# Performance work log

Measured on AMD Instinct MI355X. Metric: run time of the kernel, lower is better.

Reference implementation:

```python
import jax, jax.numpy as jnp
import numpy as np
from jax import lax

BS, C, H, W = 256, 256, 16, 16
NUM_CLASSES = 2
EPS = 1e-12  # F.normalize eps


def _l2_normalize(x):
    # F.normalize(x, dim=1, p=2): x / max(||x||_2, eps) along channel dim
    n = jnp.sqrt(jnp.sum(x * x, axis=1, keepdims=True))
    return x / jnp.maximum(n, EPS)


def _correlation(f1, f2):
    # original: (f1[:, :, None, :, :] * f2.reshape(bs,c,-1)[:, :, :, None, None]).sum(1)
    # -> [bs, h*w, h, w]; expressed as a batched contraction over channels.
    f1n = _l2_normalize(f1)                      # [bs, c, h, w]
    f2n = _l2_normalize(f2).reshape(f2.shape[0], f2.shape[1], -1)  # [bs, c, hw]
    return jnp.einsum('bcxy,bck->bkxy', f1n, f2n)


def _conv3x3(x, w, b):
    y = lax.conv_general_dilated(x, w, (1, 1), 'SAME',
                                 dimension_numbers=('NCHW', 'OIHW', 'NCHW'))
    return y + b[None, :, None, None]


def _psroi_diag(feat, num_classes, h, w):
    # full-image box, pooled==spatial, group_size==h -> each bin is one pixel:
    # out[n, c, ph, pw] = feat[n, (c*h + ph)*w + pw, ph, pw]
    bs = feat.shape[0]
    f = feat.reshape(bs, num_classes, h, w, h, w)
    f = jnp.diagonal(f, axis1=2, axis2=4)   # [bs, nc, w, w, h] (ph diag -> last)
    f = jnp.diagonal(f, axis1=2, axis2=3)   # [bs, nc, h, w]? -> [bs, nc, h_diag, w_diag]
    # after two diagonals axes are [bs, nc, ph, pw]
    return f


def setup_inputs() -> dict:
    key = jax.random.key(0)
    ks = jax.random.split(key, 5)
    std1 = float(np.sqrt(2.0 / (3 * 3 * 1024)))
    std2 = float(np.sqrt(2.0 / (3 * 3 * 512)))
    stdc = float(np.sqrt(2.0 / (1 * 1 * NUM_CLASSES * H * W)))
    return {
        'feature_1': jax.random.normal(ks[0], (BS, C, H, W), jnp.float32),
        'feature_2': jax.random.normal(ks[1], (BS, C, H, W), jnp.float32),
        'conv1_w': jax.random.normal(ks[2], (1024, 2 * (C + H * W), 3, 3), jnp.float32) * std1,
        'conv1_b': jnp.zeros((1024,), jnp.float32),
        'conv2_w': jax.random.normal(ks[3], (512, 1024, 3, 3), jnp.float32) * std2,
        'conv2_b': jnp.zeros((512,), jnp.float32),
        'conv_cls_w': jax.random.normal(ks[4], (NUM_CLASSES * H * W, 512, 1, 1), jnp.float32) * stdc,
    }


def reference(feature_1, feature_2, conv1_w, conv1_b, conv2_w, conv2_b, conv_cls_w):
    f1 = jax.nn.relu(feature_1)
    f2 = jax.nn.relu(feature_2)
    corr1 = _correlation(f1, f2)   # [bs, hw, h, w]
    corr2 = _correlation(f2, f1)
    feat = jnp.concatenate((f1, corr1, f2, corr2), axis=1)  # [bs, 2*(c+hw), h, w]
    feat = jax.nn.relu(_conv3x3(feat, conv1_w, conv1_b))
    feat = jax.nn.relu(_conv3x3(feat, conv2_w, conv2_b))
    feat = jnp.einsum('bchw,oc->bohw', feat, conv_cls_w[:, :, 0, 0])  # 1x1 conv, no bias
    feat = jax.nn.relu(feat)
    cls_base = _psroi_diag(feat, NUM_CLASSES, H, W)      # [bs, nc, h, w]
    cls_score = jnp.mean(cls_base, axis=(2, 3))          # AvgPool2d(h, w)
    cls_prob = jax.nn.softmax(cls_score, axis=1)
    # eval-mode return of the original module
    return (cls_prob, corr1, corr2)
```

## Files before the change

### kernel.cpp

```cpp
#include <hip/hip_runtime.h>


typedef __attribute__((ext_vector_type(8))) __bf16 bf16x8;
typedef __attribute__((ext_vector_type(4))) float f32x4;
typedef unsigned short u16;

template <bool B> struct BC { static constexpr bool value = B; };

__device__ __forceinline__ u16 f2bf(float f) {
  union { float f; unsigned u; } v; v.f = f;
  unsigned u = v.u;
  u += 0x7fffu + ((u >> 16) & 1u);
  return (u16)(u >> 16);
}
__device__ __forceinline__ float bf2f(u16 h) {
  union { unsigned u; float f; } v; v.u = ((unsigned)h) << 16;
  return v.f;
}
__device__ __forceinline__ void gl2lds16(const void* g, void* l) {
  __builtin_amdgcn_global_load_lds(
      (__attribute__((address_space(1))) void*)(void*)g,
      (__attribute__((address_space(3))) void*)l, 16, 0, 0);
}

__global__ __launch_bounds__(256) void k_norm(const float* __restrict__ f1,
                                              const float* __restrict__ f2,
                                              u16* __restrict__ featT,
                                              float* __restrict__ s1,
                                              float* __restrict__ s2) {
  int bx = blockIdx.x;
  int b = bx >> 2;
  int p0 = (bx & 3) << 6;
  int t = threadIdx.x;
  int p = p0 + (t & 63);
  int cg = t >> 6;
  int sp3 = ((p >> 1) & 3) << 3;
  const float* F1 = f1 + ((size_t)b << 16);
  const float* F2 = f2 + ((size_t)b << 16);
  u16* FT = featT + (((size_t)(b << 8) + p) << 10);
  float ss1 = 0.f, ss2 = 0.f;
  for (int i = 0; i < 64; ++i) {
    int c = (cg << 6) + i;
    float v1 = F1[(c << 8) + p]; v1 = v1 > 0.f ? v1 : 0.f;
    float v2 = F2[(c << 8) + p]; v2 = v2 > 0.f ? v2 : 0.f;
    ss1 += v1 * v1; ss2 += v2 * v2;
    FT[c ^ sp3] = f2bf(v1);
    FT[512 + (c ^ sp3)] = f2bf(v2);
  }
  __shared__ float l1[256], l2[256];
  l1[t] = ss1; l2[t] = ss2;
  __syncthreads();
  if (t < 64) {
    float a = l1[t] + l1[t + 64] + l1[t + 128] + l1[t + 192];
    float c2 = l2[t] + l2[t + 64] + l2[t + 128] + l2[t + 192];
    int pp = (b << 8) + p0 + t;
    s1[pp] = 1.f / fmaxf(sqrtf(a), 1e-12f);
    s2[pp] = 1.f / fmaxf(sqrtf(c2), 1e-12f);
  }
}

__global__ __launch_bounds__(256) void k_wconv(const float* __restrict__ w,
                                               u16* __restrict__ wb, int O, int C) {
  int o = blockIdx.x;
  int t = threadIdx.x;
  int sp3 = ((o >> 1) & 3) << 3;
  const float* src = w + (size_t)o * C * 9;
  for (int c = t; c < C; c += 256) {
    const float* s = src + c * 9;
    float v[9];
#pragma unroll
    for (int i = 0; i < 9; ++i) v[i] = s[i];
#pragma unroll
    for (int tap = 0; tap < 9; ++tap)
      wb[(size_t)tap * O * C + (size_t)o * C + (c ^ sp3)] = f2bf(v[tap]);
  }
}

__global__ __launch_bounds__(256) void k_corr(u16* featT,
                                              const float* __restrict__ s1,
                                              const float* __restrict__ s2,
                                              float* __restrict__ out) {
  __shared__ alignas(16) u16 Alds[128 * 32];
  __shared__ alignas(16) u16 Blds[128 * 32];
  __shared__ float tb[4][16][66];
  int bx = blockIdx.x;
  int b = bx >> 2;
  int p1b = ((bx >> 1) & 1) << 7;
  int p2b = (bx & 1) << 7;
  int t = threadIdx.x, l = t & 63, w = t >> 6;
  int wm = w >> 1, wn = w & 1, lr = l & 15, lq = l >> 4;
  int srow = (w << 4) + (l >> 2);
  int sq = (l & 3) << 3;
  int rsz = ((lq ^ ((lr >> 1) & 3)) << 3);
  const size_t bbase = (size_t)b << 18;

  f32x4 acc[4][4];
#pragma unroll
  for (int i = 0; i < 4; ++i)
#pragma unroll
    for (int j = 0; j < 4; ++j) acc[i][j] = (f32x4){0.f, 0.f, 0.f, 0.f};

#pragma unroll 1
  for (int kc = 0; kc < 8; ++kc) {
    int c0 = kc << 5;
    const u16* sA = featT + bbase + ((size_t)(p1b + srow) << 10) + (c0 + sq);
    gl2lds16(sA, Alds + ((w << 4) << 5));
    gl2lds16(sA + (64 << 10), Alds + ((64 + (w << 4)) << 5));
    const u16* sB = featT + bbase + ((size_t)(p2b + srow) << 10) + (512 + c0 + sq);
    gl2lds16(sB, Blds + ((w << 4) << 5));
    gl2lds16(sB + (64 << 10), Blds + ((64 + (w << 4)) << 5));
    __syncthreads();
    bf16x8 af[4], bfr[4];
#pragma unroll
    for (int mf = 0; mf < 4; ++mf)
      af[mf] = *(const bf16x8*)(Alds + (((wm << 6) + (mf << 4) + lr) << 5) + rsz);
#pragma unroll
    for (int nf = 0; nf < 4; ++nf)
      bfr[nf] = *(const bf16x8*)(Blds + (((wn << 6) + (nf << 4) + lr) << 5) + rsz);
#pragma unroll
    for (int mf = 0; mf < 4; ++mf)
#pragma unroll
      for (int nf = 0; nf < 4; ++nf)
        acc[mf][nf] = __builtin_amdgcn_mfma_f32_16x16x32_bf16(af[mf], bfr[nf], acc[mf][nf], 0, 0, 0);
    __syncthreads();
  }

  float sc2[4]; int p2g[4];
#pragma unroll
  for (int nf = 0; nf < 4; ++nf) {
    int p2 = p2b + (wn << 6) + (nf << 4) + lr;
    p2g[nf] = p2;
    sc2[nf] = s2[(b << 8) + p2];
  }
  float* corr1 = out + 512;
  float* corr2 = out + 512 + 16777216;
#pragma unroll
  for (int mf = 0; mf < 4; ++mf) {
    float gv[4][4];
#pragma unroll
    for (int r = 0; r < 4; ++r) {
      int p1 = p1b + (wm << 6) + (mf << 4) + (lq << 2) + r;
      float s1v = s1[(b << 8) + p1];
#pragma unroll
      for (int nf = 0; nf < 4; ++nf) gv[nf][r] = acc[mf][nf][r] * s1v * sc2[nf];
    }
#pragma unroll
    for (int r = 0; r < 4; ++r) {
      int p1 = p1b + (wm << 6) + (mf << 4) + (lq << 2) + r;
      int s1p3 = ((p1 >> 1) & 3) << 3;
#pragma unroll
      for (int nf = 0; nf < 4; ++nf) {
        corr2[((size_t)b << 16) + ((size_t)p1 << 8) + p2g[nf]] = gv[nf][r];
        featT[bbase + ((size_t)p1 << 10) + 256 + (p2g[nf] ^ s1p3)] = f2bf(gv[nf][r]);
      }
    }
#pragma unroll
    for (int r = 0; r < 4; ++r)
#pragma unroll
      for (int nf = 0; nf < 4; ++nf)
        tb[w][(lq << 2) + r][(nf << 4) + lr] = gv[nf][r];
#pragma unroll
    for (int j = 0; j < 16; ++j) {
      float v = tb[w][lr][(j << 2) + lq];
      int p2 = p2b + (wn << 6) + (j << 2) + lq;
      int s2p3 = ((p2 >> 1) & 3) << 3;
      int p1 = p1b + (wm << 6) + (mf << 4) + lr;
      corr1[((size_t)b << 16) + ((size_t)p2 << 8) + p1] = v;
      featT[bbase + ((size_t)p2 << 10) + 768 + (p1 ^ s2p3)] = f2bf(v);
    }
  }
}

template <int O, int OTB>
__global__ __launch_bounds__(512, 4) void k_conv(const u16* __restrict__ X,
                                                 const u16* __restrict__ Wb,
                                                 const float* __restrict__ bias,
                                                 u16* __restrict__ Out) {
  __shared__ alignas(16) u16 Xlds[2][260 * 32];
  __shared__ alignas(16) u16 Wlds[3][128 * 32];
  int bx = blockIdx.x;
  int otile = bx & ((1 << OTB) - 1);
  int b = bx >> OTB;
  int t = threadIdx.x, l = t & 63, w = t >> 6;
  int wm = w & 3, wn = w >> 2;
  int lr = l & 15, lq = l >> 4;
  int o0 = otile << 7;
  int srl = l >> 2;
  int sq = (l & 3) << 3;
  const size_t xbase = (size_t)b << 18;

  const u16* wsrc = Wb + (((size_t)(o0 + (w << 4) + srl)) << 10) + sq;
  const u16* xsrc0 = X + xbase + (((size_t)((w << 4) + srl)) << 10) + sq;
  const u16* xsrc1 = xsrc0 + ((size_t)128 << 10);

  u16* wdst0 = &Wlds[0][(w << 4) << 5];
  u16* wdst1 = &Wlds[1][(w << 4) << 5];
  u16* wdst2 = &Wlds[2][(w << 4) << 5];
  u16* xdA0 = &Xlds[0][(w << 4) << 5];
  u16* xdA1 = &Xlds[0][(128 + (w << 4)) << 5];
  u16* xdB0 = &Xlds[1][(w << 4) << 5];
  u16* xdB1 = &Xlds[1][(128 + (w << 4)) << 5];

  int rszw = ((lq ^ ((lr >> 1) & 3)) << 3);
  const u16* bwb0 = &Wlds[0][(((wn << 6) + lr) << 5) + rszw];
  const u16* bwb1 = &Wlds[1][(((wn << 6) + lr) << 5) + rszw];
  const u16* bwb2 = &Wlds[2][(((wn << 6) + lr) << 5) + rszw];

  int pb[4];
#pragma unroll
  for (int mf = 0; mf < 4; ++mf)
    pb[mf] = (((wm << 6) + (mf << 4) + lr) << 5);
  int xsz[3];
#pragma unroll
  for (int d = 0; d < 3; ++d)
    xsz[d] = ((lq ^ (((lr + d - 1) >> 1) & 3)) << 3);
  const int zoff = (256 << 5) + (lq << 3);

  f32x4 acc[4][4];
#pragma unroll
  for (int i = 0; i < 4; ++i)
#pragma unroll
    for (int j = 0; j < 4; ++j) acc[i][j] = (f32x4){0.f, 0.f, 0.f, 0.f};

  if (t < 32) ((unsigned*)&Xlds[t >> 4][256 << 5])[t & 15] = 0u;

  gl2lds16(xsrc0, xdA0);
  gl2lds16(xsrc1, xdA1);
  gl2lds16(wsrc, wdst0);
  gl2lds16(wsrc + ((size_t)O << 10), wdst1);
  __syncthreads();

  auto kcbody = [&](auto oddc, int kc) {
    constexpr bool ODD = decltype(oddc)::value;
    const u16* xb = ODD ? &Xlds[1][0] : &Xlds[0][0];
#pragma unroll
    for (int tap = 0; tap < 9; ++tap) {
      __builtin_amdgcn_sched_barrier(0);
      int ntap = (tap + 2) % 9;
      int nkc = kc + (tap >= 7 ? 1 : 0);
      u16* wd = ((tap + 2) % 3 == 0) ? wdst0 : (((tap + 2) % 3 == 1) ? wdst1 : wdst2);
      gl2lds16(wsrc + (size_t)ntap * ((size_t)O << 10) + (nkc << 5), wd);
      if (tap == 0) {
        if (ODD) { gl2lds16(xsrc0 + ((kc + 1) << 5), xdA0); gl2lds16(xsrc1 + ((kc + 1) << 5), xdA1); }
        else     { gl2lds16(xsrc0 + ((kc + 1) << 5), xdB0); gl2lds16(xsrc1 + ((kc + 1) << 5), xdB1); }
      }
      const u16* bwb = (tap % 3 == 0) ? bwb0 : ((tap % 3 == 1) ? bwb1 : bwb2);
      bf16x8 bwf[4];
#pragma unroll
      for (int nf = 0; nf < 4; ++nf) bwf[nf] = *(const bf16x8*)(bwb + (nf << 9));
      const int dr = tap / 3 - 1, dc = tap % 3 - 1;
      const int dpo = (((dr << 4) + dc) << 5) + xsz[dc + 1];
      bf16x8 axf[4];
#pragma unroll
      for (int mf = 0; mf < 4; ++mf) {
        int rr = (wm << 2) + mf + dr;
        bool v = ((unsigned)rr < 16u) & ((unsigned)(lr + dc) < 16u);
        int off = v ? (pb[mf] + dpo) : zoff;
        axf[mf] = *(const bf16x8*)(xb + off);
      }
#pragma unroll
      for (int mf = 0; mf < 4; ++mf)
#pragma unroll
        for (int nf = 0; nf < 4; ++nf)
          acc[mf][nf] = __builtin_amdgcn_mfma_f32_16x16x32_bf16(axf[mf], bwf[nf], acc[mf][nf], 0, 0, 0);
      if (tap == 0 || tap == 1) asm volatile("s_waitcnt vmcnt(3)" ::: "memory");
      else                      asm volatile("s_waitcnt vmcnt(1)" ::: "memory");
      __builtin_amdgcn_s_barrier();
    }
  };

#pragma unroll 1
  for (int kc2 = 0; kc2 < 16; ++kc2) {
    kcbody(BC<false>{}, 2 * kc2);
    kcbody(BC<true>{}, 2 * kc2 + 1);
  }

  __syncthreads();
  float bv[4];
#pragma unroll
  for (int nf = 0; nf < 4; ++nf) bv[nf] = bias[o0 + (wn << 6) + (nf << 4) + lr];
  u16* scr = ((u16*)Xlds) + w * 1152;
  int rr2 = l >> 2;
  int kq = l & 3;
#pragma unroll
  for (int mf = 0; mf < 4; ++mf) {
#pragma unroll
    for (int r = 0; r < 4; ++r) {
      int rr = (lq << 2) + r;
#pragma unroll
      for (int nf = 0; nf < 4; ++nf) {
        float vv = acc[mf][nf][r] + bv[nf];
        scr[rr * 72 + (nf << 4) + lr] = f2bf(vv > 0.f ? vv : 0.f);
      }
    }
    asm volatile("s_waitcnt lgkmcnt(0)" ::: "memory");
    __builtin_amdgcn_sched_barrier(0);
    int p = (wm << 6) + (mf << 4) + rr2;
    int sp = (p >> 1) & 3;
    size_t rbase = (size_t)((b << 8) + p) * O + (size_t)(o0 + (wn << 6));
#pragma unroll
    for (int j = 0; j < 2; ++j) {
      int k = (j << 2) | kq;
      int kl = (j << 2) | (kq ^ sp);
      uint4 v = *(const uint4*)(scr + rr2 * 72 + (kl << 3));
      *(uint4*)(Out + rbase + (k << 3)) = v;
    }
    asm volatile("s_waitcnt lgkmcnt(0)" ::: "memory");
    __builtin_amdgcn_sched_barrier(0);
  }
}

__global__ __launch_bounds__(256) void k_cls(const u16* __restrict__ X2,
                                             const float* __restrict__ Wc,
                                             float* __restrict__ out) {
  int b = blockIdx.x, p = threadIdx.x;
  int s = (p >> 1) & 3;
  const uint4* xv = (const uint4*)(X2 + (((size_t)(b << 8) + p) << 9));
  const float4* w0 = (const float4*)(Wc + ((size_t)p << 9));
  const float4* w1 = (const float4*)(Wc + ((size_t)(256 + p) << 9));
  float a0 = 0.f, a1 = 0.f;
#pragma unroll 4
  for (int i = 0; i < 64; ++i) {
    int ii = (i & ~3) | ((i & 3) ^ s);
    uint4 u = xv[ii];
    float x0 = bf2f((u16)(u.x & 0xffffu)), x1 = bf2f((u16)(u.x >> 16));
    float x2 = bf2f((u16)(u.y & 0xffffu)), x3 = bf2f((u16)(u.y >> 16));
    float x4 = bf2f((u16)(u.z & 0xffffu)), x5 = bf2f((u16)(u.z >> 16));
    float x6 = bf2f((u16)(u.w & 0xffffu)), x7 = bf2f((u16)(u.w >> 16));
    float4 wa = w0[i * 2], wb = w0[i * 2 + 1];
    a0 += x0 * wa.x + x1 * wa.y + x2 * wa.z + x3 * wa.w +
          x4 * wb.x + x5 * wb.y + x6 * wb.z + x7 * wb.w;
    float4 wc4 = w1[i * 2], wd = w1[i * 2 + 1];
    a1 += x0 * wc4.x + x1 * wc4.y + x2 * wc4.z + x3 * wc4.w +
          x4 * wd.x + x5 * wd.y + x6 * wd.z + x7 * wd.w;
  }
  a0 = fmaxf(a0, 0.f);
  a1 = fmaxf(a1, 0.f);
  __shared__ float r0[256], r1[256];
  r0[p] = a0; r1[p] = a1;
  for (int sdx = 128; sdx > 0; sdx >>= 1) {
    __syncthreads();
    if (p < sdx) { r0[p] += r0[p + sdx]; r1[p] += r1[p + sdx]; }
  }
  __syncthreads();
  if (p == 0) {
    float s0 = r0[0] * (1.f / 256.f), s1v = r1[0] * (1.f / 256.f);
    float m = fmaxf(s0, s1v);
    float e0 = expf(s0 - m), e1 = expf(s1v - m);
    float inv = 1.f / (e0 + e1);
    out[(b << 1) + 0] = e0 * inv;
    out[(b << 1) + 1] = e1 * inv;
  }
}

extern "C" void kernel_launch(void* const* d_in, const int* in_sizes, int n_in,
                              void* d_out, int out_size, void* d_ws, size_t ws_size,
                              hipStream_t stream) {
  const float* f1 = (const float*)d_in[0];
  const float* f2 = (const float*)d_in[1];
  const float* w1 = (const float*)d_in[2];
  const float* b1 = (const float*)d_in[3];
  const float* w2 = (const float*)d_in[4];
  const float* b2 = (const float*)d_in[5];
  const float* wc = (const float*)d_in[6];
  float* out = (float*)d_out;
  char* ws = (char*)d_ws;

  u16* featT = (u16*)(ws + 0);
  u16* out1T = (u16*)(ws + 134217728);
  u16* W1b   = (u16*)(ws + 268435456);
  u16* W2b   = (u16*)(ws + 287309824);
  float* s1  = (float*)(ws + 296747008);
  float* s2  = (float*)(ws + 297009152);
  u16* out2T = (u16*)(ws + 0);

  k_norm<<<1024, 256, 0, stream>>>(f1, f2, featT, s1, s2);
  k_wconv<<<1024, 256, 0, stream>>>(w1, W1b, 1024, 1024);
  k_wconv<<<512, 256, 0, stream>>>(w2, W2b, 512, 1024);
  k_corr<<<1024, 256, 0, stream>>>(featT, s1, s2, out);
  k_conv<1024, 3><<<2048, 512, 0, stream>>>(featT, W1b, b1, out1T);
  k_conv<512, 2><<<1024, 512, 0, stream>>>(out1T, W2b, b2, out2T);
  k_cls<<<256, 256, 0, stream>>>(out2T, wc, out);
}
```

Measured before the change: 1.902 ms.

## Switch conv kernel to 32x32x16 MFMA with 4-wave blocks and larger per-wave tiles

Rewrites the implicit-GEMM 3x3 conv kernel to use 32x32x16 bf16 MFMA instructions instead of 16x16x32, with 256-thread blocks (4 waves in a 2x2 grid) where each wave computes a 128x64 output tile. Staging loads and the LDS swizzle are reorganised to match the new fragment layout, and the epilogue is adapted to the 32x32 accumulator layout. The aim is more MFMA throughput per LDS read and fewer operand loads per FLOP. The cost is higher register pressure from 128 accumulator floats per lane and lower occupancy.

```diff
diff --git a/kernel.cpp b/kernel.cpp
--- a/kernel.cpp
+++ b/kernel.cpp
@@ -3,6 +3,7 @@
 
 typedef __attribute__((ext_vector_type(8))) __bf16 bf16x8;
 typedef __attribute__((ext_vector_type(4))) float f32x4;
+typedef __attribute__((ext_vector_type(16))) float f32x16;
 typedef unsigned short u16;
 
 template <bool B> struct BC { static constexpr bool value = B; };
@@ -172,99 +173,107 @@
 }
 
 template <int O, int OTB>
-__global__ __launch_bounds__(512, 4) void k_conv(const u16* __restrict__ X,
+__global__ __launch_bounds__(256, 2) void k_conv(const u16* __restrict__ X,
                                                  const u16* __restrict__ Wb,
                                                  const float* __restrict__ bias,
                                                  u16* __restrict__ Out) {
-  __shared__ alignas(16) u16 Xlds[2][260 * 32];
+  __shared__ alignas(16) u16 Xlds[2][257 * 32];
   __shared__ alignas(16) u16 Wlds[3][128 * 32];
   int bx = blockIdx.x;
   int otile = bx & ((1 << OTB) - 1);
   int b = bx >> OTB;
   int t = threadIdx.x, l = t & 63, w = t >> 6;
-  int wm = w & 3, wn = w >> 2;
-  int lr = l & 15, lq = l >> 4;
+  int wm = w >> 1, wn = w & 1;
+  int l31 = l & 31, l5 = l >> 5, px = l & 15;
   int o0 = otile << 7;
   int srl = l >> 2;
   int sq = (l & 3) << 3;
   const size_t xbase = (size_t)b << 18;
 
   const u16* wsrc = Wb + (((size_t)(o0 + (w << 4) + srl)) << 10) + sq;
-  const u16* xsrc0 = X + xbase + (((size_t)((w << 4) + srl)) << 10) + sq;
-  const u16* xsrc1 = xsrc0 + ((size_t)128 << 10);
-
-  u16* wdst0 = &Wlds[0][(w << 4) << 5];
-  u16* wdst1 = &Wlds[1][(w << 4) << 5];
-  u16* wdst2 = &Wlds[2][(w << 4) << 5];
-  u16* xdA0 = &Xlds[0][(w << 4) << 5];
-  u16* xdA1 = &Xlds[0][(128 + (w << 4)) << 5];
-  u16* xdB0 = &Xlds[1][(w << 4) << 5];
-  u16* xdB1 = &Xlds[1][(128 + (w << 4)) << 5];
-
-  int rszw = ((lq ^ ((lr >> 1) & 3)) << 3);
-  const u16* bwb0 = &Wlds[0][(((wn << 6) + lr) << 5) + rszw];
-  const u16* bwb1 = &Wlds[1][(((wn << 6) + lr) << 5) + rszw];
-  const u16* bwb2 = &Wlds[2][(((wn << 6) + lr) << 5) + rszw];
-
-  int pb[4];
-#pragma unroll
-  for (int mf = 0; mf < 4; ++mf)
-    pb[mf] = (((wm << 6) + (mf << 4) + lr) << 5);
-  int xsz[3];
-#pragma unroll
-  for (int d = 0; d < 3; ++d)
-    xsz[d] = ((lq ^ (((lr + d - 1) >> 1) & 3)) << 3);
-  const int zoff = (256 << 5) + (lq << 3);
-
-  f32x4 acc[4][4];
-#pragma unroll
-  for (int i = 0; i < 4; ++i)
-#pragma unroll
-    for (int j = 0; j < 4; ++j) acc[i][j] = (f32x4){0.f, 0.f, 0.f, 0.f};
+  const u16* xsrc = X + xbase + (((size_t)((w << 4) + srl)) << 10) + sq;
+
+  int czb[2][3];
+#pragma unroll
+  for (int h = 0; h < 2; ++h)
+#pragma unroll
+    for (int d = 0; d < 3; ++d)
+      czb[h][d] = (((2 * h + l5) ^ (((l31 + d - 1) >> 1) & 3)) << 4);
+  int pbase[4];
+#pragma unroll
+  for (int q = 0; q < 4; ++q)
+    pbase[q] = (((wm << 7) + (q << 5) + l31) << 6);
+  int wrow[2];
+#pragma unroll
+  for (int n = 0; n < 2; ++n)
+    wrow[n] = (((wn << 6) + (n << 5) + l31) << 6);
+  const int zo = 256 << 6;
+
+  f32x16 acc[4][2];
+#pragma unroll
+  for (int q = 0; q < 4; ++q)
+#pragma unroll
+    for (int n = 0; n < 2; ++n)
+#pragma unroll
+      for (int e = 0; e < 16; ++e) acc[q][n][e] = 0.f;
+
+  auto stageW = [&](int tap, int kc, int buf) {
+    const u16* s = wsrc + (size_t)tap * ((size_t)O << 10) + (kc << 5);
+    u16* d0 = &Wlds[buf][(w << 4) << 5];
+    gl2lds16(s, d0);
+    gl2lds16(s + ((size_t)64 << 10), d0 + (64 << 5));
+  };
+  auto stageX = [&](int kc, int buf) {
+    const u16* s = xsrc + (kc << 5);
+    u16* d0 = &Xlds[buf][(w << 4) << 5];
+#pragma unroll
+    for (int rr = 0; rr < 4; ++rr)
+      gl2lds16(s + (((size_t)rr * 64) << 10), d0 + ((rr * 64) << 5));
+  };
 
   if (t < 32) ((unsigned*)&Xlds[t >> 4][256 << 5])[t & 15] = 0u;
 
-  gl2lds16(xsrc0, xdA0);
-  gl2lds16(xsrc1, xdA1);
-  gl2lds16(wsrc, wdst0);
-  gl2lds16(wsrc + ((size_t)O << 10), wdst1);
+  stageX(0, 0);
+  stageW(0, 0, 0);
+  stageW(1, 0, 1);
   __syncthreads();
 
   auto kcbody = [&](auto oddc, int kc) {
     constexpr bool ODD = decltype(oddc)::value;
-    const u16* xb = ODD ? &Xlds[1][0] : &Xlds[0][0];
+    const char* xb = (const char*)(ODD ? &Xlds[1][0] : &Xlds[0][0]);
 #pragma unroll
     for (int tap = 0; tap < 9; ++tap) {
       __builtin_amdgcn_sched_barrier(0);
-      int ntap = (tap + 2) % 9;
-      int nkc = kc + (tap >= 7 ? 1 : 0);
-      u16* wd = ((tap + 2) % 3 == 0) ? wdst0 : (((tap + 2) % 3 == 1) ? wdst1 : wdst2);
-      gl2lds16(wsrc + (size_t)ntap * ((size_t)O << 10) + (nkc << 5), wd);
-      if (tap == 0) {
-        if (ODD) { gl2lds16(xsrc0 + ((kc + 1) << 5), xdA0); gl2lds16(xsrc1 + ((kc + 1) << 5), xdA1); }
-        else     { gl2lds16(xsrc0 + ((kc + 1) << 5), xdB0); gl2lds16(xsrc1 + ((kc + 1) << 5), xdB1); }
-      }
-      const u16* bwb = (tap % 3 == 0) ? bwb0 : ((tap % 3 == 1) ? bwb1 : bwb2);
-      bf16x8 bwf[4];
-#pragma unroll
-      for (int nf = 0; nf < 4; ++nf) bwf[nf] = *(const bf16x8*)(bwb + (nf << 9));
+      {
+        int ntap = (tap + 2 > 8) ? (tap - 7) : (tap + 2);
+        int nkc = (tap + 2 > 8) ? (kc + 1) : kc;
+        stageW(ntap, nkc, (tap + 2) % 3);
+      }
+      if (tap == 0) stageX(kc + 1, ODD ? 0 : 1);
+      const char* wbuf = (const char*)&Wlds[tap % 3][0];
       const int dr = tap / 3 - 1, dc = tap % 3 - 1;
-      const int dpo = (((dr << 4) + dc) << 5) + xsz[dc + 1];
-      bf16x8 axf[4];
-#pragma unroll
-      for (int mf = 0; mf < 4; ++mf) {
-        int rr = (wm << 2) + mf + dr;
-        bool v = ((unsigned)rr < 16u) & ((unsigned)(lr + dc) < 16u);
-        int off = v ? (pb[mf] + dpo) : zoff;
-        axf[mf] = *(const bf16x8*)(xb + off);
-      }
-#pragma unroll
-      for (int mf = 0; mf < 4; ++mf)
-#pragma unroll
-        for (int nf = 0; nf < 4; ++nf)
-          acc[mf][nf] = __builtin_amdgcn_mfma_f32_16x16x32_bf16(axf[mf], bwf[nf], acc[mf][nf], 0, 0, 0);
-      if (tap == 0 || tap == 1) asm volatile("s_waitcnt vmcnt(3)" ::: "memory");
-      else                      asm volatile("s_waitcnt vmcnt(1)" ::: "memory");
+      const int dpo = (((dr << 4) + dc) << 6);
+#pragma unroll
+      for (int h = 0; h < 2; ++h) {
+        bf16x8 bw[2], a[4];
+#pragma unroll
+        for (int n = 0; n < 2; ++n)
+          bw[n] = *(const bf16x8*)(wbuf + wrow[n] + czb[h][1]);
+#pragma unroll
+        for (int q = 0; q < 4; ++q) {
+          bool rok = (unsigned)((wm << 3) + (q << 1) + (l31 >> 4) + dr) < 16u;
+          bool cok = (unsigned)(px + dc) < 16u;
+          int off = (rok & cok) ? (pbase[q] + dpo + czb[h][dc + 1]) : zo;
+          a[q] = *(const bf16x8*)(xb + off);
+        }
+#pragma unroll
+        for (int q = 0; q < 4; ++q)
+#pragma unroll
+          for (int n = 0; n < 2; ++n)
+            acc[q][n] = __builtin_amdgcn_mfma_f32_32x32x16_bf16(a[q], bw[n], acc[q][n], 0, 0, 0);
+      }
+      if (tap == 0 || tap == 1) asm volatile("s_waitcnt vmcnt(6)" ::: "memory");
+      else                      asm volatile("s_waitcnt vmcnt(2)" ::: "memory");
       __builtin_amdgcn_s_barrier();
     }
   };
@@ -276,37 +285,41 @@
   }
 
   __syncthreads();
-  float bv[4];
-#pragma unroll
-  for (int nf = 0; nf < 4; ++nf) bv[nf] = bias[o0 + (wn << 6) + (nf << 4) + lr];
+  float bv[2];
+#pragma unroll
+  for (int n = 0; n < 2; ++n) bv[n] = bias[o0 + (wn << 6) + (n << 5) + l31];
   u16* scr = ((u16*)Xlds) + w * 1152;
-  int rr2 = l >> 2;
+  int rrow = l >> 2;
   int kq = l & 3;
-#pragma unroll
-  for (int mf = 0; mf < 4; ++mf) {
-#pragma unroll
-    for (int r = 0; r < 4; ++r) {
-      int rr = (lq << 2) + r;
-#pragma unroll
-      for (int nf = 0; nf < 4; ++nf) {
-        float vv = acc[mf][nf][r] + bv[nf];
-        scr[rr * 72 + (nf << 4) + lr] = f2bf(vv > 0.f ? vv : 0.f);
-      }
-    }
-    asm volatile("s_waitcnt lgkmcnt(0)" ::: "memory");
-    __builtin_amdgcn_sched_barrier(0);
-    int p = (wm << 6) + (mf << 4) + rr2;
-    int sp = (p >> 1) & 3;
-    size_t rbase = (size_t)((b << 8) + p) * O + (size_t)(o0 + (wn << 6));
-#pragma unroll
-    for (int j = 0; j < 2; ++j) {
-      int k = (j << 2) | kq;
-      int kl = (j << 2) | (kq ^ sp);
-      uint4 v = *(const uint4*)(scr + rr2 * 72 + (kl << 3));
-      *(uint4*)(Out + rbase + (k << 3)) = v;
-    }
-    asm volatile("s_waitcnt lgkmcnt(0)" ::: "memory");
-    __builtin_amdgcn_sched_barrier(0);
+  int lrow4 = l5 << 2;
+#pragma unroll
+  for (int q = 0; q < 4; ++q) {
+#pragma unroll
+    for (int hh = 0; hh < 2; ++hh) {
+#pragma unroll
+      for (int rr = 0; rr < 8; ++rr) {
+        int lrow = (rr & 3) + ((rr >> 2) << 3) + lrow4;
+#pragma unroll
+        for (int n = 0; n < 2; ++n) {
+          float vv = acc[q][n][hh * 8 + rr] + bv[n];
+          scr[lrow * 72 + (n << 5) + l31] = f2bf(vv > 0.f ? vv : 0.f);
+        }
+      }
+      asm volatile("s_waitcnt lgkmcnt(0)" ::: "memory");
+      __builtin_amdgcn_sched_barrier(0);
+      int p = (wm << 7) + (q << 5) + (hh << 4) + rrow;
+      int sp = (p >> 1) & 3;
+      size_t rbase = (size_t)((b << 8) + p) * O + (size_t)(o0 + (wn << 6));
+#pragma unroll
+      for (int j = 0; j < 2; ++j) {
+        int k = (j << 2) | kq;
+        int kl = (j << 2) | (kq ^ sp);
+        uint4 v = *(const uint4*)(scr + rrow * 72 + (kl << 3));
+        *(uint4*)(Out + rbase + (k << 3)) = v;
+      }
+      asm volatile("s_waitcnt lgkmcnt(0)" ::: "memory");
+      __builtin_amdgcn_sched_barrier(0);
+    }
   }
 }
 
@@ -378,7 +391,7 @@
   k_wconv<<<1024, 256, 0, stream>>>(w1, W1b, 1024, 1024);
   k_wconv<<<512, 256, 0, stream>>>(w2, W2b, 512, 1024);
   k_corr<<<1024, 256, 0, stream>>>(featT, s1, s2, out);
-  k_conv<1024, 3><<<2048, 512, 0, stream>>>(featT, W1b, b1, out1T);
-  k_conv<512, 2><<<1024, 512, 0, stream>>>(out1T, W2b, b2, out2T);
+  k_conv<1024, 3><<<2048, 256, 0, stream>>>(featT, W1b, b1, out1T);
+  k_conv<512, 2><<<1024, 256, 0, stream>>>(out1T, W2b, b2, out2T);
   k_cls<<<256, 256, 0, stream>>>(out2T, wc, out);
 }
```

Result: slower. 1.981 ms (+4.2%).

## Double-buffer LDS fragment reads in conv kernel and deepen weight prefetch

Applied to the files above, without the earlier changes.

The conv inner loop now loads the A and W fragments for the next tap from LDS into a second register set while the MFMAs for the current tap run. This hides LDS read latency behind the matrix math. The weight global-to-LDS prefetch distance grows from two taps to three, with a prologue that fills all three weight buffers. The launch-bounds occupancy hint drops from 4 to 2 to make room for the extra registers. The cls kernel also moves its XOR swizzle from the activation index to the weight index, which changes its memory access pattern.

```diff
diff --git a/kernel.cpp b/kernel.cpp
--- a/kernel.cpp
+++ b/kernel.cpp
@@ -172,7 +172,7 @@
 }
 
 template <int O, int OTB>
-__global__ __launch_bounds__(512, 4) void k_conv(const u16* __restrict__ X,
+__global__ __launch_bounds__(512, 2) void k_conv(const u16* __restrict__ X,
                                                  const u16* __restrict__ Wb,
                                                  const float* __restrict__ bias,
                                                  u16* __restrict__ Out) {
@@ -222,49 +222,76 @@
 #pragma unroll
     for (int j = 0; j < 4; ++j) acc[i][j] = (f32x4){0.f, 0.f, 0.f, 0.f};
 
+  bf16x8 fa[2][4], fw[2][4];
+
   if (t < 32) ((unsigned*)&Xlds[t >> 4][256 << 5])[t & 15] = 0u;
 
   gl2lds16(xsrc0, xdA0);
   gl2lds16(xsrc1, xdA1);
   gl2lds16(wsrc, wdst0);
   gl2lds16(wsrc + ((size_t)O << 10), wdst1);
-  __syncthreads();
+  gl2lds16(wsrc + 2 * ((size_t)O << 10), wdst2);
+  asm volatile("s_waitcnt vmcnt(1) lgkmcnt(0)" ::: "memory");
+  __builtin_amdgcn_s_barrier();
+  {
+#pragma unroll
+    for (int nf = 0; nf < 4; ++nf) fw[0][nf] = *(const bf16x8*)(bwb0 + (nf << 9));
+    const int pdpo = ((-17) << 5) + xsz[0];
+#pragma unroll
+    for (int mf = 0; mf < 4; ++mf) {
+      int rr = (wm << 2) + mf - 1;
+      bool v = ((unsigned)rr < 16u) & ((unsigned)(lr - 1) < 16u);
+      int off = v ? (pb[mf] + pdpo) : zoff;
+      fa[0][mf] = *(const bf16x8*)(&Xlds[0][0] + off);
+    }
+  }
+  asm volatile("s_waitcnt lgkmcnt(0)" ::: "memory");
+  __builtin_amdgcn_s_barrier();
 
   auto kcbody = [&](auto oddc, int kc) {
     constexpr bool ODD = decltype(oddc)::value;
     const u16* xb = ODD ? &Xlds[1][0] : &Xlds[0][0];
+    const u16* xbn = ODD ? &Xlds[0][0] : &Xlds[1][0];
 #pragma unroll
     for (int tap = 0; tap < 9; ++tap) {
+      const int CU_ = ((ODD ? 1 : 0) + tap) & 1;
+      const int NX_ = CU_ ^ 1;
       __builtin_amdgcn_sched_barrier(0);
-      int ntap = (tap + 2) % 9;
-      int nkc = kc + (tap >= 7 ? 1 : 0);
-      u16* wd = ((tap + 2) % 3 == 0) ? wdst0 : (((tap + 2) % 3 == 1) ? wdst1 : wdst2);
-      gl2lds16(wsrc + (size_t)ntap * ((size_t)O << 10) + (nkc << 5), wd);
+      {
+        int ntap = (tap + 3 > 8) ? (tap - 6) : (tap + 3);
+        int nkc = (tap >= 6) ? (kc + 1) : kc;
+        u16* wd = (tap % 3 == 0) ? wdst0 : ((tap % 3 == 1) ? wdst1 : wdst2);
+        gl2lds16(wsrc + (size_t)ntap * ((size_t)O << 10) + (nkc << 5), wd);
+      }
       if (tap == 0) {
         if (ODD) { gl2lds16(xsrc0 + ((kc + 1) << 5), xdA0); gl2lds16(xsrc1 + ((kc + 1) << 5), xdA1); }
         else     { gl2lds16(xsrc0 + ((kc + 1) << 5), xdB0); gl2lds16(xsrc1 + ((kc + 1) << 5), xdB1); }
       }
-      const u16* bwb = (tap % 3 == 0) ? bwb0 : ((tap % 3 == 1) ? bwb1 : bwb2);
-      bf16x8 bwf[4];
-#pragma unroll
-      for (int nf = 0; nf < 4; ++nf) bwf[nf] = *(const bf16x8*)(bwb + (nf << 9));
-      const int dr = tap / 3 - 1, dc = tap % 3 - 1;
-      const int dpo = (((dr << 4) + dc) << 5) + xsz[dc + 1];
-      bf16x8 axf[4];
-#pragma unroll
-      for (int mf = 0; mf < 4; ++mf) {
-        int rr = (wm << 2) + mf + dr;
-        bool v = ((unsigned)rr < 16u) & ((unsigned)(lr + dc) < 16u);
-        int off = v ? (pb[mf] + dpo) : zoff;
-        axf[mf] = *(const bf16x8*)(xb + off);
+      {
+        const int ptap = (tap == 8) ? 0 : tap + 1;
+        const u16* bwbn = ((tap + 1) % 3 == 0) ? bwb0
+                        : (((tap + 1) % 3 == 1) ? bwb1 : bwb2);
+#pragma unroll
+        for (int nf = 0; nf < 4; ++nf) fw[NX_][nf] = *(const bf16x8*)(bwbn + (nf << 9));
+        const int pdr = ptap / 3 - 1, pdc = ptap % 3 - 1;
+        const int pdpo = (((pdr << 4) + pdc) << 5) + xsz[pdc + 1];
+        const u16* xrd = (tap == 8) ? xbn : xb;
+#pragma unroll
+        for (int mf = 0; mf < 4; ++mf) {
+          int rr = (wm << 2) + mf + pdr;
+          bool v = ((unsigned)rr < 16u) & ((unsigned)(lr + pdc) < 16u);
+          int off = v ? (pb[mf] + pdpo) : zoff;
+          fa[NX_][mf] = *(const bf16x8*)(xrd + off);
+        }
       }
 #pragma unroll
       for (int mf = 0; mf < 4; ++mf)
 #pragma unroll
         for (int nf = 0; nf < 4; ++nf)
-          acc[mf][nf] = __builtin_amdgcn_mfma_f32_16x16x32_bf16(axf[mf], bwf[nf], acc[mf][nf], 0, 0, 0);
-      if (tap == 0 || tap == 1) asm volatile("s_waitcnt vmcnt(3)" ::: "memory");
-      else                      asm volatile("s_waitcnt vmcnt(1)" ::: "memory");
+          acc[mf][nf] = __builtin_amdgcn_mfma_f32_16x16x32_bf16(fa[CU_][mf], fw[CU_][nf], acc[mf][nf], 0, 0, 0);
+      asm volatile("s_waitcnt lgkmcnt(0)" ::: "memory");
+      if (tap < 2) asm volatile("s_waitcnt vmcnt(3)" ::: "memory");
+      else         asm volatile("s_waitcnt vmcnt(1)" ::: "memory");
       __builtin_amdgcn_s_barrier();
     }
   };
@@ -321,16 +348,16 @@
   float a0 = 0.f, a1 = 0.f;
 #pragma unroll 4
   for (int i = 0; i < 64; ++i) {
-    int ii = (i & ~3) | ((i & 3) ^ s);
-    uint4 u = xv[ii];
+    uint4 u = xv[i];
+    int il = (i & ~3) | ((i & 3) ^ s);
     float x0 = bf2f((u16)(u.x & 0xffffu)), x1 = bf2f((u16)(u.x >> 16));
     float x2 = bf2f((u16)(u.y & 0xffffu)), x3 = bf2f((u16)(u.y >> 16));
     float x4 = bf2f((u16)(u.z & 0xffffu)), x5 = bf2f((u16)(u.z >> 16));
     float x6 = bf2f((u16)(u.w & 0xffffu)), x7 = bf2f((u16)(u.w >> 16));
-    float4 wa = w0[i * 2], wb = w0[i * 2 + 1];
+    float4 wa = w0[il * 2], wb = w0[il * 2 + 1];
     a0 += x0 * wa.x + x1 * wa.y + x2 * wa.z + x3 * wa.w +
           x4 * wb.x + x5 * wb.y + x6 * wb.z + x7 * wb.w;
-    float4 wc4 = w1[i * 2], wd = w1[i * 2 + 1];
+    float4 wc4 = w1[il * 2], wd = w1[il * 2 + 1];
     a1 += x0 * wc4.x + x1 * wc4.y + x2 * wc4.z + x3 * wc4.w +
           x4 * wd.x + x5 * wd.y + x6 * wd.z + x7 * wd.w;
   }
```

Result: slower. 2.157 ms (+13.4%).

## Restructure conv pipeline to process two taps per barrier with double-buffered weights

Applied to the files above, without the earlier changes.

The implicit-GEMM conv main loop now handles two filter taps between barriers. It uses a 2x2 weight LDS buffer and prefetches the next two taps' weights, and the X chunk loads are scheduled at fixed sub-steps. Out-of-bounds A fragments are zeroed with a mask instead of being read from a padded zero row, which removes the LDS padding. The aim is to halve the number of barriers and wait points per K chunk. In exchange it waits with vmcnt(0) on most steps, which may expose load latency. The cls kernel also swaps which access gets the permutation: X is now read sequentially and the weight index is permuted.

```diff
diff --git a/kernel.cpp b/kernel.cpp
--- a/kernel.cpp
+++ b/kernel.cpp
@@ -176,8 +176,8 @@
                                                  const u16* __restrict__ Wb,
                                                  const float* __restrict__ bias,
                                                  u16* __restrict__ Out) {
-  __shared__ alignas(16) u16 Xlds[2][260 * 32];
-  __shared__ alignas(16) u16 Wlds[3][128 * 32];
+  __shared__ alignas(16) u16 Xlds[2][256 * 32];
+  __shared__ alignas(16) u16 Wlds[2][2][128 * 32];
   int bx = blockIdx.x;
   int otile = bx & ((1 << OTB) - 1);
   int b = bx >> OTB;
@@ -193,18 +193,14 @@
   const u16* xsrc0 = X + xbase + (((size_t)((w << 4) + srl)) << 10) + sq;
   const u16* xsrc1 = xsrc0 + ((size_t)128 << 10);
 
-  u16* wdst0 = &Wlds[0][(w << 4) << 5];
-  u16* wdst1 = &Wlds[1][(w << 4) << 5];
-  u16* wdst2 = &Wlds[2][(w << 4) << 5];
-  u16* xdA0 = &Xlds[0][(w << 4) << 5];
-  u16* xdA1 = &Xlds[0][(128 + (w << 4)) << 5];
-  u16* xdB0 = &Xlds[1][(w << 4) << 5];
-  u16* xdB1 = &Xlds[1][(128 + (w << 4)) << 5];
+  u16* xdb = &Xlds[0][0];
+  u16* wdb = &Wlds[0][0][0];
+  const int wdo = (w << 4) << 5;
+  const int xdo0 = (w << 4) << 5;
+  const int xdo1 = (128 + (w << 4)) << 5;
 
   int rszw = ((lq ^ ((lr >> 1) & 3)) << 3);
-  const u16* bwb0 = &Wlds[0][(((wn << 6) + lr) << 5) + rszw];
-  const u16* bwb1 = &Wlds[1][(((wn << 6) + lr) << 5) + rszw];
-  const u16* bwb2 = &Wlds[2][(((wn << 6) + lr) << 5) + rszw];
+  const int wro = (((wn << 6) + lr) << 5) + rszw;
 
   int pb[4];
 #pragma unroll
@@ -214,7 +210,6 @@
 #pragma unroll
   for (int d = 0; d < 3; ++d)
     xsz[d] = ((lq ^ (((lr + d - 1) >> 1) & 3)) << 3);
-  const int zoff = (256 << 5) + (lq << 3);
 
   f32x4 acc[4][4];
 #pragma unroll
@@ -222,57 +217,74 @@
 #pragma unroll
     for (int j = 0; j < 4; ++j) acc[i][j] = (f32x4){0.f, 0.f, 0.f, 0.f};
 
-  if (t < 32) ((unsigned*)&Xlds[t >> 4][256 << 5])[t & 15] = 0u;
-
-  gl2lds16(xsrc0, xdA0);
-  gl2lds16(xsrc1, xdA1);
-  gl2lds16(wsrc, wdst0);
-  gl2lds16(wsrc + ((size_t)O << 10), wdst1);
-  __syncthreads();
-
-  auto kcbody = [&](auto oddc, int kc) {
-    constexpr bool ODD = decltype(oddc)::value;
-    const u16* xb = ODD ? &Xlds[1][0] : &Xlds[0][0];
-#pragma unroll
-    for (int tap = 0; tap < 9; ++tap) {
+  gl2lds16(xsrc0, xdb + xdo0);
+  gl2lds16(xsrc1, xdb + xdo1);
+  gl2lds16(wsrc, wdb + wdo);
+  gl2lds16(wsrc + ((size_t)O << 10), wdb + 4096 + wdo);
+  asm volatile("s_waitcnt vmcnt(0)" ::: "memory");
+  __builtin_amdgcn_s_barrier();
+
+  auto sstep = [&](auto parc, int kc) {
+    constexpr int PAR = decltype(parc)::value ? 1 : 0;
+#pragma unroll
+    for (int s = 0; s < 9; ++s) {
       __builtin_amdgcn_sched_barrier(0);
-      int ntap = (tap + 2) % 9;
-      int nkc = kc + (tap >= 7 ? 1 : 0);
-      u16* wd = ((tap + 2) % 3 == 0) ? wdst0 : (((tap + 2) % 3 == 1) ? wdst1 : wdst2);
-      gl2lds16(wsrc + (size_t)ntap * ((size_t)O << 10) + (nkc << 5), wd);
-      if (tap == 0) {
-        if (ODD) { gl2lds16(xsrc0 + ((kc + 1) << 5), xdA0); gl2lds16(xsrc1 + ((kc + 1) << 5), xdA1); }
-        else     { gl2lds16(xsrc0 + ((kc + 1) << 5), xdB0); gl2lds16(xsrc1 + ((kc + 1) << 5), xdB1); }
-      }
-      const u16* bwb = (tap % 3 == 0) ? bwb0 : ((tap % 3 == 1) ? bwb1 : bwb2);
-      bf16x8 bwf[4];
-#pragma unroll
-      for (int nf = 0; nf < 4; ++nf) bwf[nf] = *(const bf16x8*)(bwb + (nf << 9));
-      const int dr = tap / 3 - 1, dc = tap % 3 - 1;
-      const int dpo = (((dr << 4) + dc) << 5) + xsz[dc + 1];
-      bf16x8 axf[4];
-#pragma unroll
-      for (int mf = 0; mf < 4; ++mf) {
-        int rr = (wm << 2) + mf + dr;
-        bool v = ((unsigned)rr < 16u) & ((unsigned)(lr + dc) < 16u);
-        int off = v ? (pb[mf] + dpo) : zoff;
-        axf[mf] = *(const bf16x8*)(xb + off);
-      }
-#pragma unroll
-      for (int mf = 0; mf < 4; ++mf)
-#pragma unroll
-        for (int nf = 0; nf < 4; ++nf)
-          acc[mf][nf] = __builtin_amdgcn_mfma_f32_16x16x32_bf16(axf[mf], bwf[nf], acc[mf][nf], 0, 0, 0);
-      if (tap == 0 || tap == 1) asm volatile("s_waitcnt vmcnt(3)" ::: "memory");
-      else                      asm volatile("s_waitcnt vmcnt(1)" ::: "memory");
+      const int wbs_rd = (PAR + s) & 1;
+      const int wbs_wr = wbs_rd ^ 1;
+#pragma unroll
+      for (int i = 0; i < 2; ++i) {
+        const int gg = 2 * s + 2 + i;
+        const int ntap = gg % 9;
+        const int dk = gg / 9;
+        gl2lds16(wsrc + (size_t)ntap * ((size_t)O << 10) + ((kc + dk) << 5),
+                 wdb + wbs_wr * 8192 + i * 4096 + wdo);
+      }
+      if (s == 0) {
+        gl2lds16(xsrc0 + ((kc + 1) << 5), xdb + 8192 + xdo0);
+        gl2lds16(xsrc1 + ((kc + 1) << 5), xdb + 8192 + xdo1);
+      }
+      if (s == 5) {
+        gl2lds16(xsrc0 + ((kc + 2) << 5), xdb + xdo0);
+        gl2lds16(xsrc1 + ((kc + 2) << 5), xdb + xdo1);
+      }
+#pragma unroll
+      for (int i = 0; i < 2; ++i) {
+        const int g = 2 * s + i;
+        const int tap = g % 9;
+        const int xpar = (g / 9) & 1;
+        const int dr = tap / 3 - 1, dc = tap % 3 - 1;
+        const u16* wr = wdb + wbs_rd * 8192 + i * 4096 + wro;
+        bf16x8 bw[4];
+#pragma unroll
+        for (int nf = 0; nf < 4; ++nf) bw[nf] = *(const bf16x8*)(wr + (nf << 9));
+        const u16* xr = xdb + xpar * 8192;
+        const int dpo = ((dr << 4) + dc) << 5;
+        bf16x8 a[4];
+#pragma unroll
+        for (int mf = 0; mf < 4; ++mf) {
+          bool ok = (((unsigned)((wm << 2) + mf + dr) < 16u) &
+                     ((unsigned)(lr + dc) < 16u));
+          int msk = ok ? -1 : 0;
+          uint4 u = *(const uint4*)(xr + ((pb[mf] + dpo + xsz[dc + 1]) & msk));
+          u.x &= msk; u.y &= msk; u.z &= msk; u.w &= msk;
+          a[mf] = *(const bf16x8*)&u;
+        }
+#pragma unroll
+        for (int mf = 0; mf < 4; ++mf)
+#pragma unroll
+          for (int nf = 0; nf < 4; ++nf)
+            acc[mf][nf] = __builtin_amdgcn_mfma_f32_16x16x32_bf16(a[mf], bw[nf], acc[mf][nf], 0, 0, 0);
+      }
+      if (s == 0 || s == 5) asm volatile("s_waitcnt vmcnt(2) lgkmcnt(0)" ::: "memory");
+      else                  asm volatile("s_waitcnt vmcnt(0) lgkmcnt(0)" ::: "memory");
       __builtin_amdgcn_s_barrier();
     }
   };
 
 #pragma unroll 1
-  for (int kc2 = 0; kc2 < 16; ++kc2) {
-    kcbody(BC<false>{}, 2 * kc2);
-    kcbody(BC<true>{}, 2 * kc2 + 1);
+  for (int S2 = 0; S2 < 8; ++S2) {
+    sstep(BC<false>{}, 4 * S2);
+    sstep(BC<true>{}, 4 * S2 + 2);
   }
 
   __syncthreads();
@@ -321,16 +333,16 @@
   float a0 = 0.f, a1 = 0.f;
 #pragma unroll 4
   for (int i = 0; i < 64; ++i) {
-    int ii = (i & ~3) | ((i & 3) ^ s);
-    uint4 u = xv[ii];
+    uint4 u = xv[i];
+    int il = (i & ~3) | ((i & 3) ^ s);
     float x0 = bf2f((u16)(u.x & 0xffffu)), x1 = bf2f((u16)(u.x >> 16));
     float x2 = bf2f((u16)(u.y & 0xffffu)), x3 = bf2f((u16)(u.y >> 16));
     float x4 = bf2f((u16)(u.z & 0xffffu)), x5 = bf2f((u16)(u.z >> 16));
     float x6 = bf2f((u16)(u.w & 0xffffu)), x7 = bf2f((u16)(u.w >> 16));
-    float4 wa = w0[i * 2], wb = w0[i * 2 + 1];
+    float4 wa = w0[il * 2], wb = w0[il * 2 + 1];
     a0 += x0 * wa.x + x1 * wa.y + x2 * wa.z + x3 * wa.w +
           x4 * wb.x + x5 * wb.y + x6 * wb.z + x7 * wb.w;
-    float4 wc4 = w1[i * 2], wd = w1[i * 2 + 1];
+    float4 wc4 = w1[il * 2], wd = w1[il * 2 + 1];
     a1 += x0 * wc4.x + x1 * wc4.y + x2 * wc4.z + x3 * wc4.w +
           x4 * wd.x + x5 * wd.y + x6 * wd.z + x7 * wd.w;
   }
```

New measurement: 2.490 ms. +30.9%, slower.
